# Kernel tuning notes

Measured on AMD Instinct MI355X. Metric: run time of the kernel, lower is better.

## Reference

```python
import jax, jax.numpy as jnp
import numpy as np

N_NODES = 100000
N_EDGES = 3200000
IN_F = 256
OUT_F = 128
NEG_SLOPE = 0.2


def setup_inputs() -> dict:
    key = jax.random.key(0)
    k1, k2, k3, k4, k5 = jax.random.split(key, 5)
    features = jax.random.normal(k1, (N_NODES, IN_F), dtype=jnp.float32)
    # xavier-uniform-ish linear weight [out, in]
    limit = float(np.sqrt(6.0 / (IN_F + OUT_F)))
    weight = jax.random.uniform(k2, (OUT_F, IN_F), dtype=jnp.float32, minval=-limit, maxval=limit)
    edge_vals = jax.random.uniform(k3, (N_EDGES,), dtype=jnp.float32)
    edge_rows = jax.random.randint(k4, (N_EDGES,), 0, N_NODES, dtype=jnp.int32)
    edge_cols = jax.random.randint(k5, (N_EDGES,), 0, N_NODES, dtype=jnp.int32)
    return {"features": features, "weight": weight, "edge_vals": edge_vals,
            "edge_rows": edge_rows, "edge_cols": edge_cols}


def reference(features, weight, edge_vals, edge_rows, edge_cols):
    # support = LeakyReLU(features @ W^T)   (active=True path)
    support = jax.nn.leaky_relu(jnp.einsum('ni,oi->no', features, weight), NEG_SLOPE)
    # output = spmm(adj, support): out[r] += v_e * support[c_e]
    gathered = support[edge_cols] * edge_vals[:, None]   # [E, out]
    out = jax.ops.segment_sum(gathered, edge_rows, num_segments=N_NODES)
    return out
```

## Files before the change

### kernel.cpp

```cpp
#include <hip/hip_runtime.h>
#include <hip/hip_bf16.h>

#define N_NODES 100000
#define N_EDGES 3200000
#define IN_F 256
#define OUT_F 128
#define NEG_SLOPE 0.2f
#define NB 782
#define CHUNK 4096
#define NPB 782
#define BCAP 4608
#define CURSTRIDE 16

typedef short s16x8 __attribute__((ext_vector_type(8)));
typedef float f32x4 __attribute__((ext_vector_type(4)));
typedef float f32x2v __attribute__((ext_vector_type(2)));
typedef unsigned u32x2 __attribute__((ext_vector_type(2)));

__device__ __forceinline__ unsigned short f2bf(float f) {
    __bf16 h = (__bf16)f;
    return __builtin_bit_cast(unsigned short, h);
}
__device__ __forceinline__ float bf2f(unsigned short u) {
    unsigned int x = ((unsigned int)u) << 16;
    return __builtin_bit_cast(float, x);
}

__global__ void wcvt_kernel(const float* __restrict__ w, unsigned short* __restrict__ wb) {
    int t = blockIdx.x * blockDim.x + threadIdx.x;
    if (t >= (OUT_F / 16) * (IN_F / 32) * 64) return;
    int lane = t & 63;
    int nt   = (t >> 6) & 7;
    int kit  = t >> 9;
    int l16  = lane & 15;
    int quad = lane >> 4;
    const float* src = w + (nt * 16 + l16) * IN_F + kit * 32 + quad * 8;
    float4 v0 = *(const float4*)src;
    float4 v1 = *(const float4*)(src + 4);
    ushort4 o0, o1;
    o0.x = f2bf(v0.x); o0.y = f2bf(v0.y); o0.z = f2bf(v0.z); o0.w = f2bf(v0.w);
    o1.x = f2bf(v1.x); o1.y = f2bf(v1.y); o1.z = f2bf(v1.z); o1.w = f2bf(v1.w);
    *(ushort4*)(wb + t * 8)     = o0;
    *(ushort4*)(wb + t * 8 + 4) = o1;
}

__global__ __launch_bounds__(256) void gemm_kernel(
    const float* __restrict__ feat, const unsigned short* __restrict__ wb,
    unsigned short* __restrict__ sup) {
    int wid  = threadIdx.x >> 6;
    int lane = threadIdx.x & 63;
    long m0 = ((long)blockIdx.x * 4 + wid) * 16;
    if (m0 >= N_NODES) return;
    int quad = lane >> 4;
    int l16  = lane & 15;
    int kq   = quad * 8;

    const float* arow = feat + (m0 + l16) * IN_F + kq;

    f32x4 acc[8];
#pragma unroll
    for (int nt = 0; nt < 8; ++nt) acc[nt] = (f32x4){0.f, 0.f, 0.f, 0.f};

#pragma unroll
    for (int k0 = 0; k0 < IN_F; k0 += 32) {
        f32x4 a0 = __builtin_nontemporal_load((const f32x4*)(arow + k0));
        f32x4 a1 = __builtin_nontemporal_load((const f32x4*)(arow + k0 + 4));
        s16x8 a;
        a[0] = (short)f2bf(a0[0]); a[1] = (short)f2bf(a0[1]);
        a[2] = (short)f2bf(a0[2]); a[3] = (short)f2bf(a0[3]);
        a[4] = (short)f2bf(a1[0]); a[5] = (short)f2bf(a1[1]);
        a[6] = (short)f2bf(a1[2]); a[7] = (short)f2bf(a1[3]);
        const unsigned short* wp = wb + (k0 >> 5) * 4096 + lane * 8;
#pragma unroll
        for (int nt = 0; nt < 8; ++nt) {
            s16x8 b = *(const s16x8*)(wp + nt * 512);
            acc[nt] = __builtin_amdgcn_mfma_f32_16x16x32_bf16(a, b, acc[nt], 0, 0, 0);
        }
    }

    int crow = (int)m0 + quad * 4;
#pragma unroll
    for (int nt = 0; nt < 8; ++nt) {
#pragma unroll
        for (int r = 0; r < 4; ++r) {
            float v = acc[nt][r];
            v = (v > 0.f) ? v : (NEG_SLOPE * v);
            sup[(long)(crow + r) * OUT_F + nt * 16 + l16] = f2bf(v);
        }
    }
}

__global__ __launch_bounds__(256) void mscatter_kernel(const int* __restrict__ rows,
    const int* __restrict__ cols, const float* __restrict__ vals,
    int* __restrict__ cursor, uint2* __restrict__ ed) {
    __shared__ uint2 stage[CHUNK];
    __shared__ unsigned short sbkt[CHUNK];
    __shared__ int lhist[NB];
    __shared__ int lbase[NB];
    __shared__ int st[256];
    int t = threadIdx.x;
    for (int s = t; s < NB; s += 256) lhist[s] = 0;
    __syncthreads();
    int e0 = blockIdx.x * CHUNK;
    int m = N_EDGES - e0; if (m > CHUNK) m = CHUNK;

    int rk[16]; int rr[16]; unsigned cw[16], vw[16];
#pragma unroll
    for (int k = 0; k < 16; ++k) {
        int i = k * 256 + t;
        if (i < m) {
            int e = e0 + i;
            int r = __builtin_nontemporal_load(rows + e);
            rr[k] = r;
            cw[k] = (unsigned)__builtin_nontemporal_load(cols + e);
            vw[k] = __builtin_bit_cast(unsigned, __builtin_nontemporal_load(vals + e));
            rk[k] = atomicAdd(&lhist[r >> 7], 1);
        }
    }
    __syncthreads();
    for (int s = t; s < NB; s += 256) {
        int c = lhist[s];
        if (c) lbase[s] = atomicAdd(&cursor[s * CURSTRIDE], c);
    }
    int base = t * 4; int sum = 0; int hv[4];
#pragma unroll
    for (int k = 0; k < 4; ++k) {
        int s = base + k;
        hv[k] = (s < NB) ? lhist[s] : 0;
        sum += hv[k];
    }
    st[t] = sum;
    __syncthreads();
    for (int o = 1; o < 256; o <<= 1) {
        int x = (t >= o) ? st[t - o] : 0;
        __syncthreads();
        st[t] += x;
        __syncthreads();
    }
    int run = st[t] - sum;
#pragma unroll
    for (int k = 0; k < 4; ++k) {
        int s = base + k;
        if (s < NB) lhist[s] = run;
        run += hv[k];
    }
    __syncthreads();
#pragma unroll
    for (int k = 0; k < 16; ++k) {
        int i = k * 256 + t;
        if (i < m) {
            int r  = rr[k];
            int b  = r >> 7;
            int rl = r & 127;
            int pos = lhist[b] + rk[k];
            stage[pos].x = ((unsigned)rl << 17) | cw[k];
            stage[pos].y = vw[k];
            sbkt[pos] = (unsigned short)b;
        }
    }
    __syncthreads();
    for (int i = t; i < m; i += 256) {
        int b = sbkt[i];
        int g = lbase[b] + (i - lhist[b]);
        if (g < BCAP) ed[(long)b * BCAP + g] = stage[i];
    }
}

__global__ __launch_bounds__(1024) void gather_kernel(const uint2* __restrict__ ed,
    const int* __restrict__ cursor,
    const unsigned short* __restrict__ sup, float* __restrict__ out, int b0) {
    __shared__ uint2 stage[BCAP];
    __shared__ int h[128];
    __shared__ int bs[128];
    __shared__ int cur[128];
    int t = threadIdx.x;
    int bkt = b0 + blockIdx.x;
    if (t < 128) h[t] = 0;
    __syncthreads();
    int n = cursor[bkt * CURSTRIDE]; if (n > BCAP) n = BCAP;
    const uint2* p = ed + (long)bkt * BCAP;

    uint2 er[5];
#pragma unroll
    for (int k = 0; k < 5; ++k) {
        int i = k * 1024 + t;
        if (i < n) {
            u32x2 v = __builtin_nontemporal_load((const u32x2*)(p + i));
            er[k].x = v[0]; er[k].y = v[1];
        }
    }
#pragma unroll
    for (int k = 0; k < 5; ++k) {
        int i = k * 1024 + t;
        if (i < n) atomicAdd(&h[er[k].x >> 17], 1);
    }
    __syncthreads();

    if (t < 128) bs[t] = h[t];
    __syncthreads();
    for (int o = 1; o < 128; o <<= 1) {
        int v = 0;
        if (t < 128 && t >= o) v = bs[t - o];
        __syncthreads();
        if (t < 128) bs[t] += v;
        __syncthreads();
    }
    if (t < 128) {
        int excl = bs[t] - h[t];
        bs[t] = excl;
        cur[t] = excl;
    }
    __syncthreads();

#pragma unroll
    for (int k = 0; k < 5; ++k) {
        int i = k * 1024 + t;
        if (i < n) {
            int rl = er[k].x >> 17;
            int pos = atomicAdd(&cur[rl], 1);
            stage[pos] = er[k];
        }
    }
    __syncthreads();

    int wid = t >> 6, lane = t & 63;
    long rowbase = (long)bkt * 128;

#define PROC(E) {                                                            \
        int col = (E).x & 0x1FFFF;                                           \
        float v = __builtin_bit_cast(float, (E).y);                          \
        ushort2 s2 = *(const ushort2*)(sup + (long)col * OUT_F + lane * 2);  \
        a0 += v * bf2f(s2.x); a1 += v * bf2f(s2.y);                          \
    }

    for (int rq = 0; rq < 8; ++rq) {
        int lr = wid * 8 + rq;
        int s0 = bs[lr];
        int mm = h[lr];
        float a0 = 0.f, a1 = 0.f;
        int i = 0;
        for (; i + 16 <= mm; i += 16) {
            uint2 e[16];
#pragma unroll
            for (int k = 0; k < 16; ++k) e[k] = stage[s0 + i + k];
#pragma unroll
            for (int k = 0; k < 16; ++k) PROC(e[k]);
        }
        for (; i + 8 <= mm; i += 8) {
            uint2 e0 = stage[s0 + i],     e1 = stage[s0 + i + 1];
            uint2 e2 = stage[s0 + i + 2], e3 = stage[s0 + i + 3];
            uint2 e4 = stage[s0 + i + 4], e5 = stage[s0 + i + 5];
            uint2 e6 = stage[s0 + i + 6], e7 = stage[s0 + i + 7];
            PROC(e0); PROC(e1); PROC(e2); PROC(e3);
            PROC(e4); PROC(e5); PROC(e6); PROC(e7);
        }
        for (; i < mm; ++i) { uint2 e0 = stage[s0 + i]; PROC(e0); }
        long grow = rowbase + lr;
        if (grow < N_NODES) {
            f32x2v f; f[0] = a0; f[1] = a1;
            __builtin_nontemporal_store(f, (f32x2v*)(out + grow * OUT_F + lane * 2));
        }
    }
#undef PROC
}

extern "C" void kernel_launch(void* const* d_in, const int* in_sizes, int n_in,
                              void* d_out, int out_size, void* d_ws, size_t ws_size,
                              hipStream_t stream) {
    const float* feat  = (const float*)d_in[0];
    const float* w     = (const float*)d_in[1];
    const float* evals = (const float*)d_in[2];
    const int*   erows = (const int*)d_in[3];
    const int*   ecols = (const int*)d_in[4];
    float* out = (float*)d_out;

    char* p = (char*)d_ws;
    unsigned short* wb  = (unsigned short*)p;  p += 65536;
    unsigned short* sup = (unsigned short*)p;  p += (size_t)N_NODES * OUT_F * 2;
    int* cursor = (int*)p;                     p += (size_t)NB * CURSTRIDE * 4;
    uint2* ed   = (uint2*)p;

    hipMemsetAsync(cursor, 0, (size_t)NB * CURSTRIDE * 4, stream);

    wcvt_kernel<<<16, 256, 0, stream>>>(w, wb);

    int gemm_blocks = (N_NODES / 16 + 3) / 4;
    gemm_kernel<<<gemm_blocks, 256, 0, stream>>>(feat, wb, sup);

    mscatter_kernel<<<NPB, 256, 0, stream>>>(erows, ecols, evals, cursor, ed);

    int gh = NB / 2;
    gather_kernel<<<gh, 1024, 0, stream>>>(ed, cursor, sup, out, 0);
    gather_kernel<<<NB - gh, 1024, 0, stream>>>(ed, cursor, sup, out, gh);
}
```

Baseline: 407.9 us.

## Replace global atomic bucket cursors with deterministic histogram and prefix-scan offsets

Adds a separate histogram pass over edge rows and a per-bucket scan across blocks, so each scatter block reads a precomputed offset per bucket instead of doing global atomicAdds on shared cursors. This removes global atomic contention and the cursor memset, and makes edge placement deterministic. In exchange it adds two kernel launches, an extra read of the row array, and a count matrix of about 2.4 MB that is written and read back.

```diff
diff --git a/kernel.cpp b/kernel.cpp
--- a/kernel.cpp
+++ b/kernel.cpp
@@ -10,7 +10,6 @@
 #define CHUNK 4096
 #define NPB 782
 #define BCAP 4608
-#define CURSTRIDE 16
 
 typedef short s16x8 __attribute__((ext_vector_type(8)));
 typedef float f32x4 __attribute__((ext_vector_type(4)));
@@ -90,9 +89,54 @@
     }
 }
 
+__global__ __launch_bounds__(256) void hist_kernel(const int* __restrict__ rows,
+                                                   int* __restrict__ gcnt) {
+    __shared__ int lh[NB];
+    int t = threadIdx.x;
+    for (int s = t; s < NB; s += 256) lh[s] = 0;
+    __syncthreads();
+    int e0 = blockIdx.x * CHUNK;
+    int m = N_EDGES - e0; if (m > CHUNK) m = CHUNK;
+    for (int k = t; k < m; k += 256)
+        atomicAdd(&lh[__builtin_nontemporal_load(rows + e0 + k) >> 7], 1);
+    __syncthreads();
+    for (int s = t; s < NB; s += 256)
+        gcnt[s * NPB + blockIdx.x] = lh[s];
+}
+
+__global__ __launch_bounds__(256) void scan_kernel(int* __restrict__ gcnt,
+                                                   int* __restrict__ bcnt) {
+    __shared__ int st[256];
+    int s = blockIdx.x, t = threadIdx.x;
+    int* row = gcnt + (long)s * NPB;
+    int v[4]; int sum = 0;
+#pragma unroll
+    for (int k = 0; k < 4; ++k) {
+        int i = t * 4 + k;
+        v[k] = (i < NPB) ? row[i] : 0;
+        sum += v[k];
+    }
+    st[t] = sum;
+    __syncthreads();
+    for (int o = 1; o < 256; o <<= 1) {
+        int x = (t >= o) ? st[t - o] : 0;
+        __syncthreads();
+        st[t] += x;
+        __syncthreads();
+    }
+    int run = st[t] - sum;
+#pragma unroll
+    for (int k = 0; k < 4; ++k) {
+        int i = t * 4 + k;
+        if (i < NPB) row[i] = run;
+        run += v[k];
+    }
+    if (t == 255) bcnt[s] = run;
+}
+
 __global__ __launch_bounds__(256) void mscatter_kernel(const int* __restrict__ rows,
     const int* __restrict__ cols, const float* __restrict__ vals,
-    int* __restrict__ cursor, uint2* __restrict__ ed) {
+    const int* __restrict__ boff, uint2* __restrict__ ed) {
     __shared__ uint2 stage[CHUNK];
     __shared__ unsigned short sbkt[CHUNK];
     __shared__ int lhist[NB];
@@ -118,10 +162,8 @@
         }
     }
     __syncthreads();
-    for (int s = t; s < NB; s += 256) {
-        int c = lhist[s];
-        if (c) lbase[s] = atomicAdd(&cursor[s * CURSTRIDE], c);
-    }
+    for (int s = t; s < NB; s += 256)
+        lbase[s] = boff[(long)s * NPB + blockIdx.x];
     int base = t * 4; int sum = 0; int hv[4];
 #pragma unroll
     for (int k = 0; k < 4; ++k) {
@@ -167,7 +209,7 @@
 }
 
 __global__ __launch_bounds__(1024) void gather_kernel(const uint2* __restrict__ ed,
-    const int* __restrict__ cursor,
+    const int* __restrict__ bcnt,
     const unsigned short* __restrict__ sup, float* __restrict__ out, int b0) {
     __shared__ uint2 stage[BCAP];
     __shared__ int h[128];
@@ -177,7 +219,7 @@
     int bkt = b0 + blockIdx.x;
     if (t < 128) h[t] = 0;
     __syncthreads();
-    int n = cursor[bkt * CURSTRIDE]; if (n > BCAP) n = BCAP;
+    int n = bcnt[bkt]; if (n > BCAP) n = BCAP;
     const uint2* p = ed + (long)bkt * BCAP;
 
     uint2 er[5];
@@ -277,19 +319,20 @@
     char* p = (char*)d_ws;
     unsigned short* wb  = (unsigned short*)p;  p += 65536;
     unsigned short* sup = (unsigned short*)p;  p += (size_t)N_NODES * OUT_F * 2;
-    int* cursor = (int*)p;                     p += (size_t)NB * CURSTRIDE * 4;
+    int* gcnt   = (int*)p;                     p += (size_t)NB * NPB * 4;
+    int* bcnt   = (int*)p;                     p += 4096;
     uint2* ed   = (uint2*)p;
-
-    hipMemsetAsync(cursor, 0, (size_t)NB * CURSTRIDE * 4, stream);
 
     wcvt_kernel<<<16, 256, 0, stream>>>(w, wb);
 
     int gemm_blocks = (N_NODES / 16 + 3) / 4;
     gemm_kernel<<<gemm_blocks, 256, 0, stream>>>(feat, wb, sup);
 
-    mscatter_kernel<<<NPB, 256, 0, stream>>>(erows, ecols, evals, cursor, ed);
+    hist_kernel<<<NPB, 256, 0, stream>>>(erows, gcnt);
+    scan_kernel<<<NB, 256, 0, stream>>>(gcnt, bcnt);
+    mscatter_kernel<<<NPB, 256, 0, stream>>>(erows, ecols, evals, gcnt, ed);
 
     int gh = NB / 2;
-    gather_kernel<<<gh, 1024, 0, stream>>>(ed, cursor, sup, out, 0);
-    gather_kernel<<<NB - gh, 1024, 0, stream>>>(ed, cursor, sup, out, gh);
-}
+    gather_kernel<<<gh, 1024, 0, stream>>>(ed, bcnt, sup, out, 0);
+    gather_kernel<<<NB - gh, 1024, 0, stream>>>(ed, bcnt, sup, out, gh);
+}
```

Result: faster. 388.4 us (-4.8%).
